# Kernel optimization log

Hardware: AMD Instinct MI355X
Metric: run time of the kernel (lower is better)

The kernel has to match this reference:

```python
import jax, jax.numpy as jnp
import numpy as np

B, N, D = 8, 2048, 1024
DC = 1024          # d_center
K = 4              # num_centers
NUM_JUMPS = 2
SPAN = 2
FIN = (2 + 2 * NUM_JUMPS + 1) * D  # 7*D

def _gelu(x):
    return jax.nn.gelu(x, approximate=False)  # torch nn.GELU default is exact erf

def setup_inputs() -> dict:
    key = jax.random.key(0)
    ks = jax.random.split(key, 16)
    s = lambda k, *sh: jax.random.normal(k, sh, dtype=jnp.float32) * 0.02
    return {
        "queries": jax.random.normal(ks[0], (B, N, D), dtype=jnp.float32),
        "fr_w1": s(ks[1], FIN, D), "fr_b1": jnp.zeros((D,), jnp.float32),
        "fr_w2": s(ks[2], D, D),   "fr_b2": jnp.zeros((D,), jnp.float32),
        "tc_w1": s(ks[3], D, DC),  "tc_b1": jnp.zeros((DC,), jnp.float32),
        "tc_w2": s(ks[4], DC, DC), "tc_b2": jnp.zeros((DC,), jnp.float32),
        "centers": jax.random.normal(ks[5], (K, DC), dtype=jnp.float32),
        "fc_w1": s(ks[6], D + DC, D), "fc_b1": jnp.zeros((D,), jnp.float32),
        "fc_w2": s(ks[7], D, D),      "fc_b2": jnp.zeros((D,), jnp.float32),
        "g_w": s(ks[8], D + DC, D),   "g_b": jnp.zeros((D,), jnp.float32),
    }

def reference(queries, fr_w1, fr_b1, fr_w2, fr_b2,
              tc_w1, tc_b1, tc_w2, tc_b2, centers,
              fc_w1, fc_b1, fc_w2, fc_b2, g_w, g_b):
    x = queries
    shifts = [1, -1, 0]  # left, right, x
    for i in range(1, NUM_JUMPS + 1):
        shifts += [i * SPAN, -i * SPAN]
    fusion = jnp.concatenate([jnp.roll(x, s, axis=1) for s in shifts], axis=-1)  # [B,N,7D]
    x_ring = _gelu(fusion @ fr_w1 + fr_b1) @ fr_w2 + fr_b2                       # [B,N,D]
    token_proj = _gelu(x_ring @ tc_w1 + tc_b1) @ tc_w2 + tc_b2                   # [B,N,DC]
    w = jax.nn.softmax(jnp.einsum('bnd,kd->bnk', token_proj, centers), axis=-1)  # [B,N,K]
    weighted = jnp.einsum('bnk,kd->bnd', w, centers)                             # [B,N,DC]
    fus2 = jnp.concatenate([x_ring, weighted], axis=-1)                          # [B,N,D+DC]
    gate = jax.nn.sigmoid(fus2 @ g_w + g_b)
    fc = _gelu(fus2 @ fc_w1 + fc_b1) @ fc_w2 + fc_b2
    return gate * fc + (1.0 - gate) * x_ring
```

## Files before the change

kernel.cpp:

```cpp
#include <hip/hip_runtime.h>
#include <hip/hip_bf16.h>
#include <math.h>

typedef unsigned short u16;
typedef __attribute__((ext_vector_type(8))) short short8;
typedef __attribute__((ext_vector_type(4))) float f32x4;


__device__ __forceinline__ float bf2f(u16 b) {
  return __uint_as_float(((unsigned int)b) << 16);
}
__device__ __forceinline__ u16 f2bf(float f) {
  unsigned int u = __float_as_uint(f);
  u += 0x7FFFu + ((u >> 16) & 1u);
  return (u16)(u >> 16);
}
__device__ __forceinline__ float gelu_exact(float x) {
  return 0.5f * x * (1.0f + erff(x * 0.70710678118654752f));
}

__device__ __forceinline__ void cp16(const void* g, void* l) {
  __builtin_amdgcn_global_load_lds(
      (const __attribute__((address_space(1))) unsigned int*)g,
      (__attribute__((address_space(3))) unsigned int*)l, 16, 0, 0);
}

template <int MODE, bool GATHER>
__global__ __launch_bounds__(256) void gemm128(
    const u16* __restrict__ A, int lda, const u16* __restrict__ Wt, int K,
    const float* __restrict__ bias, const float* __restrict__ bias2,
    void* __restrict__ out0, int ldo0, void* __restrict__ out1,
    void* __restrict__ out2, const float* __restrict__ p0,
    const float* __restrict__ p1, const float* __restrict__ p2) {
  __shared__ __align__(16) u16 As[128 * 64];
  __shared__ __align__(16) u16 Bs[128 * 64];

  const int tid = threadIdx.x;
  const int lane = tid & 63;
  const int wave = tid >> 6;
  const int wm = wave >> 1;
  const int wn = wave & 1;

  const unsigned linear = blockIdx.y * gridDim.x + blockIdx.x;
  const unsigned xcd = linear & 7u;
  const unsigned pos = linear >> 3;
  const unsigned bx = pos % gridDim.x;
  const unsigned by = xcd * (gridDim.y >> 3) + pos / gridDim.x;
  const int m0 = by * 128;
  const int n0 = bx * 128;

  const int srow = lane >> 3;
  const int sq = lane & 7;
  const int sqs = sq ^ srow;

  f32x4 acc[4][4];
#pragma unroll
  for (int i = 0; i < 4; i++)
#pragma unroll
    for (int j = 0; j < 4; j++) acc[i][j] = (f32x4){0.f, 0.f, 0.f, 0.f};

  for (int k0 = 0; k0 < K; k0 += 64) {
#pragma unroll
    for (int i = 0; i < 4; i++) {
      const int rloc = wave * 32 + i * 8 + srow;
      long gofs;
      if (GATHER) {
        const int seg = k0 >> 10;
        int shift;
        switch (seg) {
          case 0: shift = 1; break;
          case 1: shift = -1; break;
          case 2: shift = 0; break;
          case 3: shift = 2; break;
          case 4: shift = -2; break;
          case 5: shift = 4; break;
          default: shift = -4; break;
        }
        const int m = m0 + rloc;
        const int b = m >> 11;
        const int nsrc = ((m & 2047) - shift) & 2047;
        gofs = (long)((b << 11) | nsrc) * 1024 + (k0 & 1023) + sqs * 8;
      } else {
        gofs = (long)(m0 + rloc) * lda + k0 + sqs * 8;
      }
      cp16(A + gofs, &As[(wave * 32 + i * 8) * 64]);
    }
#pragma unroll
    for (int i = 0; i < 4; i++) {
      const int rloc = wave * 32 + i * 8 + srow;
      const long gofs = (long)(n0 + rloc) * K + k0 + sqs * 8;
      cp16(Wt + gofs, &Bs[(wave * 32 + i * 8) * 64]);
    }
    __syncthreads();

    const int q4 = lane >> 4;
    const int r16 = lane & 15;
#pragma unroll
    for (int kk = 0; kk < 2; kk++) {
      short8 af[4], bf[4];
#pragma unroll
      for (int mi = 0; mi < 4; mi++) {
        const int row = wm * 64 + mi * 16 + r16;
        const int q = (kk * 4 + q4) ^ (row & 7);
        af[mi] = *(const short8*)&As[row * 64 + q * 8];
      }
#pragma unroll
      for (int ni = 0; ni < 4; ni++) {
        const int row = wn * 64 + ni * 16 + r16;
        const int q = (kk * 4 + q4) ^ (row & 7);
        bf[ni] = *(const short8*)&Bs[row * 64 + q * 8];
      }
#pragma unroll
      for (int mi = 0; mi < 4; mi++)
#pragma unroll
        for (int ni = 0; ni < 4; ni++)
          acc[mi][ni] = __builtin_amdgcn_mfma_f32_16x16x32_bf16(
              af[mi], bf[ni], acc[mi][ni], 0, 0, 0);
    }
    __syncthreads();
  }

  const int ccol = lane & 15;
  const int crow = (lane >> 4) * 4;
#pragma unroll
  for (int mi = 0; mi < 4; mi++) {
#pragma unroll
    for (int r = 0; r < 4; r++) {
      const int m = m0 + wm * 64 + mi * 16 + crow + r;
      float4 wrow;
      if (MODE == 8) wrow = *(const float4*)(p0 + (size_t)m * 4);
#pragma unroll
      for (int ni = 0; ni < 4; ni++) {
        const int n = n0 + wn * 64 + ni * 16 + ccol;
        const float v = acc[mi][ni][r];
        if (MODE == 0) {
          ((u16*)out0)[(long)m * ldo0 + n] = f2bf(gelu_exact(v + bias[n]));
        } else if (MODE == 4) {
          const float g = p0[(long)m * 1024 + n];
          const float xr = p1[(long)m * 1024 + n];
          ((float*)out0)[(long)m * ldo0 + n] =
              g * (v + bias[n]) + (1.0f - g) * xr;
        } else if (MODE == 6) {
          ((u16*)out0)[(long)m * ldo0 + n] = f2bf(v);
        } else if (MODE == 7) {
          if (n < 1024) {
            const float s = v + bias[n];
            ((float*)out1)[(long)m * 1024 + n] = s;
            ((u16*)out0)[(long)m * 1024 + n] = f2bf(s);
          } else {
            const int nn = n - 1024;
            ((u16*)out2)[(long)m * 1024 + nn] = f2bf(gelu_exact(v + bias2[nn]));
          }
        } else if (MODE == 8) {
          if (n < 1024) {
            const float4 g2 = *(const float4*)(p1 + (size_t)n * 4);
            const float s = v + bias[n] + wrow.x * g2.x + wrow.y * g2.y +
                            wrow.z * g2.z + wrow.w * g2.w;
            ((float*)out0)[(long)m * 1024 + n] = 1.0f / (1.0f + expf(-s));
          } else {
            const int nn = n - 1024;
            const float4 f2 = *(const float4*)(p2 + (size_t)nn * 4);
            const float s = v + bias2[nn] + wrow.x * f2.x + wrow.y * f2.y +
                            wrow.z * f2.z + wrow.w * f2.w;
            ((u16*)out1)[(long)m * 1024 + nn] = f2bf(gelu_exact(s));
          }
        }
      }
    }
  }
}

__global__ __launch_bounds__(256) void cast_bf16(const float* __restrict__ in,
                                                 u16* __restrict__ out, int n4) {
  const long i = (long)blockIdx.x * 256 + threadIdx.x;
  if (i < n4) {
    const float4 v = ((const float4*)in)[i];
    ushort4 o;
    o.x = f2bf(v.x); o.y = f2bf(v.y); o.z = f2bf(v.z); o.w = f2bf(v.w);
    ((ushort4*)out)[i] = o;
  }
}

__global__ __launch_bounds__(256) void transp_bf16(const float* __restrict__ in,
                                                   u16* __restrict__ out, int K,
                                                   int N) {
  __shared__ float tile[32][33];
  const int tx = threadIdx.x & 31;
  const int ty = threadIdx.x >> 5;
  const long r0 = (long)blockIdx.y * 32;
  const long c0 = (long)blockIdx.x * 32;
#pragma unroll
  for (int r = 0; r < 4; r++)
    tile[ty + r * 8][tx] = in[(r0 + ty + r * 8) * N + c0 + tx];
  __syncthreads();
#pragma unroll
  for (int r = 0; r < 4; r++)
    out[(c0 + ty + r * 8) * K + r0 + tx] = f2bf(tile[tx][ty + r * 8]);
}

__global__ __launch_bounds__(256) void fold_all(
    const u16* __restrict__ GbT, const u16* __restrict__ FbT,
    const u16* __restrict__ Wt3, const float* __restrict__ centers,
    const float* __restrict__ fr_b2, const float* __restrict__ tc_b1,
    const float* __restrict__ tc_w2, const float* __restrict__ tc_b2,
    float* __restrict__ G2T, float* __restrict__ F2T, float* __restrict__ c2,
    float* __restrict__ S, float* __restrict__ bc) {
  const int b = blockIdx.x;
  const int wave = threadIdx.x >> 6, lane = threadIdx.x & 63;
  if (b < 256) {
    const int n = b * 4 + wave;
    float g[4] = {0.f, 0.f, 0.f, 0.f}, f[4] = {0.f, 0.f, 0.f, 0.f};
#pragma unroll
    for (int p = 0; p < 2; p++) {
      const int base = p * 512 + lane * 8;
      const short8 gv = *(const short8*)(GbT + (long)n * 1024 + base);
      const short8 fv = *(const short8*)(FbT + (long)n * 1024 + base);
#pragma unroll
      for (int e = 0; e < 8; e++) {
        const float ge = bf2f((u16)gv[e]), fe = bf2f((u16)fv[e]);
#pragma unroll
        for (int k = 0; k < 4; k++) {
          const float c = centers[k * 1024 + base + e];
          g[k] += ge * c;
          f[k] += fe * c;
        }
      }
    }
#pragma unroll
    for (int k = 0; k < 4; k++)
#pragma unroll
      for (int off = 32; off > 0; off >>= 1) {
        g[k] += __shfl_xor(g[k], off);
        f[k] += __shfl_xor(f[k], off);
      }
    if (lane == 0) {
#pragma unroll
      for (int k = 0; k < 4; k++) {
        G2T[n * 4 + k] = g[k];
        F2T[n * 4 + k] = f[k];
      }
    }
  } else if (b < 512) {
    const int j = (b - 256) * 4 + wave;
    float s = 0.f;
#pragma unroll
    for (int p = 0; p < 2; p++) {
      const int base = p * 512 + lane * 8;
      const short8 wv = *(const short8*)(Wt3 + (long)j * 1024 + base);
#pragma unroll
      for (int e = 0; e < 8; e++) s += fr_b2[base + e] * bf2f((u16)wv[e]);
    }
#pragma unroll
    for (int off = 32; off > 0; off >>= 1) s += __shfl_xor(s, off);
    if (lane == 0) c2[j] = s + tc_b1[j];
  } else if (b < 768) {
    const int d = (b - 512) * 4 + wave;
    const float* row = tc_w2 + (long)d * 1024;
    float s0 = 0.f, s1 = 0.f, s2 = 0.f, s3 = 0.f;
    for (int e = lane; e < 1024; e += 64) {
      const float w = row[e];
      s0 += w * centers[e];
      s1 += w * centers[1024 + e];
      s2 += w * centers[2048 + e];
      s3 += w * centers[3072 + e];
    }
#pragma unroll
    for (int off = 32; off > 0; off >>= 1) {
      s0 += __shfl_xor(s0, off);
      s1 += __shfl_xor(s1, off);
      s2 += __shfl_xor(s2, off);
      s3 += __shfl_xor(s3, off);
    }
    if (lane == 0) {
      S[d] = s0; S[1024 + d] = s1; S[2048 + d] = s2; S[3072 + d] = s3;
    }
  } else {
    const int k = wave;
    float s = 0.f;
    for (int e = lane; e < 1024; e += 64) s += tc_b2[e] * centers[k * 1024 + e];
#pragma unroll
    for (int off = 32; off > 0; off >>= 1) s += __shfl_xor(s, off);
    if (lane == 0) bc[k] = s;
  }
}

__global__ __launch_bounds__(256) void centers_kernel(
    const u16* __restrict__ h2, const float* __restrict__ S,
    const float* __restrict__ bc, float* __restrict__ wtok) {
  const int lane = threadIdx.x & 63;
  const int wave = threadIdx.x >> 6;
  const long t = (long)blockIdx.x * 4 + wave;
  const u16* row = h2 + t * 1024;
  float d0 = 0.f, d1 = 0.f, d2 = 0.f, d3 = 0.f;
#pragma unroll
  for (int j = 0; j < 2; j++) {
    const int dbase = j * 512 + lane * 8;
    const short8 v = *(const short8*)(row + dbase);
#pragma unroll
    for (int e = 0; e < 8; e++) {
      const float x = bf2f((u16)v[e]);
      const int d = dbase + e;
      d0 += x * S[d];
      d1 += x * S[1024 + d];
      d2 += x * S[2048 + d];
      d3 += x * S[3072 + d];
    }
  }
#pragma unroll
  for (int off = 32; off > 0; off >>= 1) {
    d0 += __shfl_xor(d0, off);
    d1 += __shfl_xor(d1, off);
    d2 += __shfl_xor(d2, off);
    d3 += __shfl_xor(d3, off);
  }
  if (lane == 0) {
    d0 += bc[0]; d1 += bc[1]; d2 += bc[2]; d3 += bc[3];
    const float mx = fmaxf(fmaxf(d0, d1), fmaxf(d2, d3));
    float e0 = expf(d0 - mx), e1 = expf(d1 - mx), e2 = expf(d2 - mx),
          e3 = expf(d3 - mx);
    const float inv = 1.0f / (e0 + e1 + e2 + e3);
    *(float4*)(wtok + t * 4) = (float4){e0 * inv, e1 * inv, e2 * inv, e3 * inv};
  }
}

extern "C" void kernel_launch(void* const* d_in, const int* in_sizes, int n_in,
                              void* d_out, int out_size, void* d_ws,
                              size_t ws_size, hipStream_t stream) {
  const float* queries = (const float*)d_in[0];
  const float* fr_w1 = (const float*)d_in[1];
  const float* fr_b1 = (const float*)d_in[2];
  const float* fr_w2 = (const float*)d_in[3];
  const float* fr_b2 = (const float*)d_in[4];
  const float* tc_w1 = (const float*)d_in[5];
  const float* tc_b1 = (const float*)d_in[6];
  const float* tc_w2 = (const float*)d_in[7];
  const float* tc_b2 = (const float*)d_in[8];
  const float* centers = (const float*)d_in[9];
  const float* fc_w1 = (const float*)d_in[10];
  const float* fc_b1 = (const float*)d_in[11];
  const float* fc_w2 = (const float*)d_in[12];
  const float* fc_b2 = (const float*)d_in[13];
  const float* g_w = (const float*)d_in[14];
  const float* g_b = (const float*)d_in[15];

  char* ws = (char*)d_ws;
  u16* Wt1 = (u16*)ws; ws += (size_t)7168 * 1024 * 2;
  u16* Wt3 = (u16*)ws; ws += (size_t)1024 * 1024 * 2;
  u16* Wt6 = (u16*)ws; ws += (size_t)1024 * 1024 * 2;
  u16* WtJ = (u16*)ws; ws += (size_t)2048 * 1024 * 2;
  u16* WtG2 = (u16*)ws; ws += (size_t)2048 * 1024 * 2;
  u16* Fw2b = (u16*)ws; ws += (size_t)1024 * 1024 * 2;
  u16* GbT = (u16*)ws; ws += (size_t)1024 * 1024 * 2;
  u16* FbT = (u16*)ws; ws += (size_t)1024 * 1024 * 2;
  u16* Xb = (u16*)ws;  ws += (size_t)16384 * 1024 * 2;
  u16* h1 = (u16*)ws;  ws += (size_t)16384 * 1024 * 2;
  u16* xrb = (u16*)ws; ws += (size_t)16384 * 1024 * 2;
  float* xring = (float*)ws; ws += (size_t)16384 * 1024 * 4;
  float* wtok = (float*)ws; ws += (size_t)16384 * 4 * 4;
  float* S = (float*)ws; ws += (size_t)4 * 1024 * 4;
  float* G2T = (float*)ws; ws += (size_t)1024 * 4 * 4;
  float* F2T = (float*)ws; ws += (size_t)1024 * 4 * 4;
  float* c2 = (float*)ws; ws += (size_t)1024 * 4;
  float* bc = (float*)ws; ws += 16;
  float* gate = (float*)d_out;
  float* out = (float*)d_out;

  cast_bf16<<<16384, 256, 0, stream>>>(queries, Xb, 16384 * 1024 / 4);
  cast_bf16<<<1024, 256, 0, stream>>>(fr_w2, Fw2b, 1024 * 1024 / 4);
  transp_bf16<<<dim3(32, 224), 256, 0, stream>>>(fr_w1, Wt1, 7168, 1024);
  transp_bf16<<<dim3(32, 32), 256, 0, stream>>>(tc_w1, Wt3, 1024, 1024);
  transp_bf16<<<dim3(32, 32), 256, 0, stream>>>(fc_w2, Wt6, 1024, 1024);
  transp_bf16<<<dim3(32, 32), 256, 0, stream>>>(fr_w2, WtJ, 1024, 1024);
  transp_bf16<<<dim3(32, 32), 256, 0, stream>>>(g_w, WtG2, 1024, 1024);
  transp_bf16<<<dim3(32, 32), 256, 0, stream>>>(fc_w1,
                                                WtG2 + (size_t)1024 * 1024,
                                                1024, 1024);
  transp_bf16<<<dim3(32, 32), 256, 0, stream>>>(g_w + (size_t)1024 * 1024, GbT,
                                                1024, 1024);
  transp_bf16<<<dim3(32, 32), 256, 0, stream>>>(fc_w1 + (size_t)1024 * 1024,
                                                FbT, 1024, 1024);
  fold_all<<<769, 256, 0, stream>>>(GbT, FbT, Wt3, centers, fr_b2, tc_b1,
                                    tc_w2, tc_b2, G2T, F2T, c2, S, bc);
  gemm128<6, false><<<dim3(8, 8), 256, 0, stream>>>(
      Wt3, 1024, Fw2b, 1024, nullptr, nullptr, WtJ + (size_t)1024 * 1024, 1024,
      nullptr, nullptr, nullptr, nullptr, nullptr);

  gemm128<0, true><<<dim3(8, 128), 256, 0, stream>>>(
      Xb, 0, Wt1, 7168, fr_b1, nullptr, h1, 1024, nullptr, nullptr, nullptr,
      nullptr, nullptr);
  gemm128<7, false><<<dim3(16, 128), 256, 0, stream>>>(
      h1, 1024, WtJ, 1024, fr_b2, c2, xrb, 1024, xring, Xb, nullptr, nullptr,
      nullptr);
  centers_kernel<<<4096, 256, 0, stream>>>(Xb, S, bc, wtok);
  gemm128<8, false><<<dim3(16, 128), 256, 0, stream>>>(
      xrb, 1024, WtG2, 1024, g_b, fc_b1, gate, 1024, h1, nullptr, wtok, G2T,
      F2T);
  gemm128<4, false><<<dim3(8, 128), 256, 0, stream>>>(
      h1, 1024, Wt6, 1024, fc_b2, nullptr, out, 1024, nullptr, nullptr, gate,
      xring, nullptr);
}
```

Measured before the change: 863.9 us.

## Replace main GEMMs with 256x256 tile, 8-wave, 4-stage pipelined kernel

Moves the four large GEMMs onto a new 256x256-tile kernel with 512 threads and 128KB of dynamic LDS. The kernel uses a 4-deep ring buffer of 32-wide K slices loaded with global_load_lds and interleaves async loads with MFMA phases, using explicit waitcnt, barriers and setprio. The goal is to raise arithmetic intensity per block and hide global-load latency that the old single-buffered 128x128 kernel exposed. In exchange it allows only one block per CU and leaves fewer blocks for wave-quantization balance. The hand-written barriers and waitcnts also carry correctness risk.

New measurement: 817.3 us. 5.4% less time.

```diff
diff --git a/kernel.cpp b/kernel.cpp
--- a/kernel.cpp
+++ b/kernel.cpp
@@ -26,46 +26,54 @@
 }
 
 template <int MODE, bool GATHER>
-__global__ __launch_bounds__(256) void gemm128(
+__global__ __launch_bounds__(512) void gemm256(
     const u16* __restrict__ A, int lda, const u16* __restrict__ Wt, int K,
     const float* __restrict__ bias, const float* __restrict__ bias2,
     void* __restrict__ out0, int ldo0, void* __restrict__ out1,
     void* __restrict__ out2, const float* __restrict__ p0,
     const float* __restrict__ p1, const float* __restrict__ p2) {
-  __shared__ __align__(16) u16 As[128 * 64];
-  __shared__ __align__(16) u16 Bs[128 * 64];
-
+  extern __shared__ __align__(16) char sm[];
   const int tid = threadIdx.x;
   const int lane = tid & 63;
   const int wave = tid >> 6;
-  const int wm = wave >> 1;
-  const int wn = wave & 1;
+  const int wm = wave >> 2;
+  const int wn = wave & 3;
 
   const unsigned linear = blockIdx.y * gridDim.x + blockIdx.x;
   const unsigned xcd = linear & 7u;
   const unsigned pos = linear >> 3;
   const unsigned bx = pos % gridDim.x;
   const unsigned by = xcd * (gridDim.y >> 3) + pos / gridDim.x;
-  const int m0 = by * 128;
-  const int n0 = bx * 128;
-
-  const int srow = lane >> 3;
-  const int sq = lane & 7;
-  const int sqs = sq ^ srow;
-
-  f32x4 acc[4][4];
-#pragma unroll
-  for (int i = 0; i < 4; i++)
+  const int m0 = by * 256;
+  const int n0 = bx * 256;
+
+  const int sl = lane >> 3;
+  const int qqs = (lane & 7) ^ sl;
+  const int rowoff = sl * 2 + (qqs >> 2);
+  const int colq = qqs & 3;
+
+  const int r16 = lane & 15, q4 = lane >> 4;
+  const int qqr = (((r16 & 1) << 2) | q4) ^ (r16 >> 1);
+  const int laneA = wm * 8192 + (r16 >> 1) * 128 + qqr * 16;
+  const int laneB = wn * 4096 + (r16 >> 1) * 128 + qqr * 16;
+
+  const int nt = K >> 5;
+
+  f32x4 acc[8][4];
+#pragma unroll
+  for (int i = 0; i < 8; i++)
 #pragma unroll
     for (int j = 0; j < 4; j++) acc[i][j] = (f32x4){0.f, 0.f, 0.f, 0.f};
 
-  for (int k0 = 0; k0 < K; k0 += 64) {
-#pragma unroll
-    for (int i = 0; i < 4; i++) {
-      const int rloc = wave * 32 + i * 8 + srow;
+  auto stage_A = [&](int sdst, int ssrc) {
+#pragma unroll
+    for (int i = 0; i < 2; i++) {
+      const int chunk = wave + i * 8;
+      const int row = chunk * 16 + rowoff;
       long gofs;
       if (GATHER) {
-        const int seg = k0 >> 10;
+        const int kg = ssrc * 32 + colq * 8;
+        const int seg = kg >> 10;
         int shift;
         switch (seg) {
           case 0: shift = 1; break;
@@ -76,57 +84,84 @@
           case 5: shift = 4; break;
           default: shift = -4; break;
         }
-        const int m = m0 + rloc;
+        const int m = m0 + row;
         const int b = m >> 11;
         const int nsrc = ((m & 2047) - shift) & 2047;
-        gofs = (long)((b << 11) | nsrc) * 1024 + (k0 & 1023) + sqs * 8;
+        gofs = (long)((b << 11) | nsrc) * 1024 + (kg & 1023);
       } else {
-        gofs = (long)(m0 + rloc) * lda + k0 + sqs * 8;
-      }
-      cp16(A + gofs, &As[(wave * 32 + i * 8) * 64]);
-    }
-#pragma unroll
-    for (int i = 0; i < 4; i++) {
-      const int rloc = wave * 32 + i * 8 + srow;
-      const long gofs = (long)(n0 + rloc) * K + k0 + sqs * 8;
-      cp16(Wt + gofs, &Bs[(wave * 32 + i * 8) * 64]);
-    }
-    __syncthreads();
-
-    const int q4 = lane >> 4;
-    const int r16 = lane & 15;
-#pragma unroll
-    for (int kk = 0; kk < 2; kk++) {
-      short8 af[4], bf[4];
-#pragma unroll
-      for (int mi = 0; mi < 4; mi++) {
-        const int row = wm * 64 + mi * 16 + r16;
-        const int q = (kk * 4 + q4) ^ (row & 7);
-        af[mi] = *(const short8*)&As[row * 64 + q * 8];
-      }
-#pragma unroll
-      for (int ni = 0; ni < 4; ni++) {
-        const int row = wn * 64 + ni * 16 + r16;
-        const int q = (kk * 4 + q4) ^ (row & 7);
-        bf[ni] = *(const short8*)&Bs[row * 64 + q * 8];
-      }
-#pragma unroll
-      for (int mi = 0; mi < 4; mi++)
-#pragma unroll
-        for (int ni = 0; ni < 4; ni++)
-          acc[mi][ni] = __builtin_amdgcn_mfma_f32_16x16x32_bf16(
-              af[mi], bf[ni], acc[mi][ni], 0, 0, 0);
-    }
-    __syncthreads();
-  }
+        gofs = (long)(m0 + row) * lda + ssrc * 32 + colq * 8;
+      }
+      cp16(A + gofs, sm + (sdst & 3) * 32768 + chunk * 1024);
+    }
+  };
+  auto stage_B = [&](int sdst, int ssrc) {
+#pragma unroll
+    for (int i = 0; i < 2; i++) {
+      const int chunk = wave + i * 8;
+      const int row = chunk * 16 + rowoff;
+      const long gofs = (long)(n0 + row) * K + ssrc * 32 + colq * 8;
+      cp16(Wt + gofs, sm + (sdst & 3) * 32768 + 16384 + chunk * 1024);
+    }
+  };
+
+  stage_A(0, 0); stage_B(0, 0);
+  stage_A(1, 1); stage_B(1, 1);
+  stage_A(2, 2); stage_B(2, 2);
+  asm volatile("s_waitcnt vmcnt(8)" ::: "memory");
+  __builtin_amdgcn_s_barrier();
+
+  for (int s = 0; s < nt; ++s) {
+    const int s3 = (s + 3 < nt) ? s + 3 : nt - 1;
+    const char* abase = sm + (s & 3) * 32768;
+    short8 af[4], bf[4];
+
+#pragma unroll
+    for (int ni = 0; ni < 4; ni++)
+      bf[ni] = *(const short8*)(abase + 16384 + laneB + ni * 1024);
+#pragma unroll
+    for (int mi = 0; mi < 4; mi++)
+      af[mi] = *(const short8*)(abase + laneA + mi * 1024);
+    stage_A(s + 3, s3);
+    __builtin_amdgcn_s_barrier();
+    asm volatile("s_waitcnt lgkmcnt(0)" ::: "memory");
+    __builtin_amdgcn_sched_barrier(0);
+    __builtin_amdgcn_s_setprio(1);
+#pragma unroll
+    for (int mi = 0; mi < 4; mi++)
+#pragma unroll
+      for (int ni = 0; ni < 4; ni++)
+        acc[mi][ni] = __builtin_amdgcn_mfma_f32_16x16x32_bf16(
+            af[mi], bf[ni], acc[mi][ni], 0, 0, 0);
+    __builtin_amdgcn_s_setprio(0);
+    __builtin_amdgcn_s_barrier();
+
+#pragma unroll
+    for (int mi = 0; mi < 4; mi++)
+      af[mi] = *(const short8*)(abase + laneA + 4096 + mi * 1024);
+    stage_B(s + 3, s3);
+    asm volatile("s_waitcnt vmcnt(8)" ::: "memory");
+    __builtin_amdgcn_s_barrier();
+    asm volatile("s_waitcnt lgkmcnt(0)" ::: "memory");
+    __builtin_amdgcn_sched_barrier(0);
+    __builtin_amdgcn_s_setprio(1);
+#pragma unroll
+    for (int mi = 0; mi < 4; mi++)
+#pragma unroll
+      for (int ni = 0; ni < 4; ni++)
+        acc[4 + mi][ni] = __builtin_amdgcn_mfma_f32_16x16x32_bf16(
+            af[mi], bf[ni], acc[4 + mi][ni], 0, 0, 0);
+    __builtin_amdgcn_s_setprio(0);
+    __builtin_amdgcn_s_barrier();
+  }
+  asm volatile("s_waitcnt vmcnt(0)" ::: "memory");
 
   const int ccol = lane & 15;
   const int crow = (lane >> 4) * 4;
 #pragma unroll
-  for (int mi = 0; mi < 4; mi++) {
+  for (int mi = 0; mi < 8; mi++) {
 #pragma unroll
     for (int r = 0; r < 4; r++) {
-      const int m = m0 + wm * 64 + mi * 16 + crow + r;
+      const int m = m0 + wm * 128 + mi * 16 + crow + r;
       float4 wrow;
       if (MODE == 8) wrow = *(const float4*)(p0 + (size_t)m * 4);
 #pragma unroll
@@ -170,6 +205,120 @@
   }
 }
 
+template <int MODE, bool GATHER>
+__global__ __launch_bounds__(256) void gemm128(
+    const u16* __restrict__ A, int lda, const u16* __restrict__ Wt, int K,
+    const float* __restrict__ bias, const float* __restrict__ bias2,
+    void* __restrict__ out0, int ldo0, void* __restrict__ out1,
+    void* __restrict__ out2, const float* __restrict__ p0,
+    const float* __restrict__ p1, const float* __restrict__ p2) {
+  __shared__ __align__(16) u16 As[128 * 64];
+  __shared__ __align__(16) u16 Bs[128 * 64];
+
+  const int tid = threadIdx.x;
+  const int lane = tid & 63;
+  const int wave = tid >> 6;
+  const int wm = wave >> 1;
+  const int wn = wave & 1;
+
+  const unsigned linear = blockIdx.y * gridDim.x + blockIdx.x;
+  const unsigned xcd = linear & 7u;
+  const unsigned pos = linear >> 3;
+  const unsigned bx = pos % gridDim.x;
+  const unsigned by = xcd * (gridDim.y >> 3) + pos / gridDim.x;
+  const int m0 = by * 128;
+  const int n0 = bx * 128;
+
+  const int srow = lane >> 3;
+  const int sq = lane & 7;
+  const int sqs = sq ^ srow;
+
+  f32x4 acc[4][4];
+#pragma unroll
+  for (int i = 0; i < 4; i++)
+#pragma unroll
+    for (int j = 0; j < 4; j++) acc[i][j] = (f32x4){0.f, 0.f, 0.f, 0.f};
+
+  for (int k0 = 0; k0 < K; k0 += 64) {
+#pragma unroll
+    for (int i = 0; i < 4; i++) {
+      const int rloc = wave * 32 + i * 8 + srow;
+      long gofs;
+      if (GATHER) {
+        const int seg = k0 >> 10;
+        int shift;
+        switch (seg) {
+          case 0: shift = 1; break;
+          case 1: shift = -1; break;
+          case 2: shift = 0; break;
+          case 3: shift = 2; break;
+          case 4: shift = -2; break;
+          case 5: shift = 4; break;
+          default: shift = -4; break;
+        }
+        const int m = m0 + rloc;
+        const int b = m >> 11;
+        const int nsrc = ((m & 2047) - shift) & 2047;
+        gofs = (long)((b << 11) | nsrc) * 1024 + (k0 & 1023) + sqs * 8;
+      } else {
+        gofs = (long)(m0 + rloc) * lda + k0 + sqs * 8;
+      }
+      cp16(A + gofs, &As[(wave * 32 + i * 8) * 64]);
+    }
+#pragma unroll
+    for (int i = 0; i < 4; i++) {
+      const int rloc = wave * 32 + i * 8 + srow;
+      const long gofs = (long)(n0 + rloc) * K + k0 + sqs * 8;
+      cp16(Wt + gofs, &Bs[(wave * 32 + i * 8) * 64]);
+    }
+    __syncthreads();
+
+    const int q4 = lane >> 4;
+    const int r16 = lane & 15;
+#pragma unroll
+    for (int kk = 0; kk < 2; kk++) {
+      short8 af[4], bf[4];
+#pragma unroll
+      for (int mi = 0; mi < 4; mi++) {
+        const int row = wm * 64 + mi * 16 + r16;
+        const int q = (kk * 4 + q4) ^ (row & 7);
+        af[mi] = *(const short8*)&As[row * 64 + q * 8];
+      }
+#pragma unroll
+      for (int ni = 0; ni < 4; ni++) {
+        const int row = wn * 64 + ni * 16 + r16;
+        const int q = (kk * 4 + q4) ^ (row & 7);
+        bf[ni] = *(const short8*)&Bs[row * 64 + q * 8];
+      }
+#pragma unroll
+      for (int mi = 0; mi < 4; mi++)
+#pragma unroll
+        for (int ni = 0; ni < 4; ni++)
+          acc[mi][ni] = __builtin_amdgcn_mfma_f32_16x16x32_bf16(
+              af[mi], bf[ni], acc[mi][ni], 0, 0, 0);
+    }
+    __syncthreads();
+  }
+
+  const int ccol = lane & 15;
+  const int crow = (lane >> 4) * 4;
+#pragma unroll
+  for (int mi = 0; mi < 4; mi++) {
+#pragma unroll
+    for (int r = 0; r < 4; r++) {
+      const int m = m0 + wm * 64 + mi * 16 + crow + r;
+#pragma unroll
+      for (int ni = 0; ni < 4; ni++) {
+        const int n = n0 + wn * 64 + ni * 16 + ccol;
+        const float v = acc[mi][ni][r];
+        if (MODE == 6) {
+          ((u16*)out0)[(long)m * ldo0 + n] = f2bf(v);
+        }
+      }
+    }
+  }
+}
+
 __global__ __launch_bounds__(256) void cast_bf16(const float* __restrict__ in,
                                                  u16* __restrict__ out, int n4) {
   const long i = (long)blockIdx.x * 256 + threadIdx.x;
@@ -365,6 +514,23 @@
   float* gate = (float*)d_out;
   float* out = (float*)d_out;
 
+  static bool attr_set = false;
+  if (!attr_set) {
+    attr_set = true;
+    (void)hipFuncSetAttribute((const void*)gemm256<0, true>,
+                              hipFuncAttributeMaxDynamicSharedMemorySize,
+                              131072);
+    (void)hipFuncSetAttribute((const void*)gemm256<7, false>,
+                              hipFuncAttributeMaxDynamicSharedMemorySize,
+                              131072);
+    (void)hipFuncSetAttribute((const void*)gemm256<8, false>,
+                              hipFuncAttributeMaxDynamicSharedMemorySize,
+                              131072);
+    (void)hipFuncSetAttribute((const void*)gemm256<4, false>,
+                              hipFuncAttributeMaxDynamicSharedMemorySize,
+                              131072);
+  }
+
   cast_bf16<<<16384, 256, 0, stream>>>(queries, Xb, 16384 * 1024 / 4);
   cast_bf16<<<1024, 256, 0, stream>>>(fr_w2, Fw2b, 1024 * 1024 / 4);
   transp_bf16<<<dim3(32, 224), 256, 0, stream>>>(fr_w1, Wt1, 7168, 1024);
@@ -385,17 +551,17 @@
       Wt3, 1024, Fw2b, 1024, nullptr, nullptr, WtJ + (size_t)1024 * 1024, 1024,
       nullptr, nullptr, nullptr, nullptr, nullptr);
 
-  gemm128<0, true><<<dim3(8, 128), 256, 0, stream>>>(
+  gemm256<0, true><<<dim3(4, 64), 512, 131072, stream>>>(
       Xb, 0, Wt1, 7168, fr_b1, nullptr, h1, 1024, nullptr, nullptr, nullptr,
       nullptr, nullptr);
-  gemm128<7, false><<<dim3(16, 128), 256, 0, stream>>>(
+  gemm256<7, false><<<dim3(8, 64), 512, 131072, stream>>>(
       h1, 1024, WtJ, 1024, fr_b2, c2, xrb, 1024, xring, Xb, nullptr, nullptr,
       nullptr);
   centers_kernel<<<4096, 256, 0, stream>>>(Xb, S, bc, wtok);
-  gemm128<8, false><<<dim3(16, 128), 256, 0, stream>>>(
+  gemm256<8, false><<<dim3(8, 64), 512, 131072, stream>>>(
       xrb, 1024, WtG2, 1024, g_b, fc_b1, gate, 1024, h1, nullptr, wtok, G2T,
       F2T);
-  gemm128<4, false><<<dim3(8, 128), 256, 0, stream>>>(
+  gemm256<4, false><<<dim3(4, 64), 512, 131072, stream>>>(
       h1, 1024, Wt6, 1024, fc_b2, nullptr, out, 1024, nullptr, nullptr, gate,
       xring, nullptr);
 }
```
